# Performance work log

Hardware: AMD Instinct MI355X
Metric: run time of the kernel (lower is better)

Reference implementation:

```python
import jax, jax.numpy as jnp
import numpy as np

N = 100000   # nodes
E = 50000    # hyperedges
K = 4        # nodes per hyperedge
D = 128      # out_dim (= in_dim here)
ED = 64      # edge_dim
H = 8        # num_heads


def _build_pairs(seed=0):
    # Sparse equivalent of the incidence-matrix nested loops:
    # for each edge e with member set S, emit ordered pairs (v, e, u) for v,u in S.
    rng = np.random.default_rng(seed)
    cover = rng.permutation(N).reshape(N // K, K)          # guarantees every node owns >=1 pair group
    rand = rng.integers(0, N, size=(E - N // K, K))
    edge_nodes = np.concatenate([cover, rand], axis=0)      # [E, K]
    owners = np.repeat(edge_nodes, K, axis=1).ravel()       # v, repeated K times per edge slot
    pair_u = np.tile(edge_nodes, (1, K)).ravel()            # u, tiled
    pair_e = np.repeat(np.arange(E), K * K)
    return owners.astype(np.int32), pair_e.astype(np.int32), pair_u.astype(np.int32)


def setup_inputs() -> dict:
    key = jax.random.key(0)
    ks = jax.random.split(key, 12)
    owners, pair_e, pair_u = _build_pairs()
    s = 0.05
    return {
        "x": jax.random.normal(ks[0], (N, D), jnp.float32),
        "edge_attr": jax.random.normal(ks[1], (E, ED), jnp.float32),
        "w_lin": jax.random.normal(ks[2], (D, D), jnp.float32) * s,   # self.lin (no bias)
        "w_e": jax.random.normal(ks[3], (ED, D), jnp.float32) * s,    # self.edge_lin (no bias)
        "w_q": jax.random.normal(ks[4], (D, D), jnp.float32) * s,
        "b_q": jax.random.normal(ks[5], (D,), jnp.float32) * s,
        "w_k": jax.random.normal(ks[6], (D, D), jnp.float32) * s,
        "b_k": jax.random.normal(ks[7], (D,), jnp.float32) * s,
        "w_v": jax.random.normal(ks[8], (D, D), jnp.float32) * s,
        "b_v": jax.random.normal(ks[9], (D,), jnp.float32) * s,
        "w_o": jax.random.normal(ks[10], (D, D), jnp.float32) * s,
        "b_o": jax.random.normal(ks[11], (D,), jnp.float32) * s,
        "owners": jnp.asarray(owners),
        "pair_e": jnp.asarray(pair_e),
        "pair_u": jnp.asarray(pair_u),
    }


def reference(x, edge_attr, w_lin, w_e, w_q, b_q, w_k, b_k, w_v, b_v, w_o, b_o, owners, pair_e, pair_u):
    n = x.shape[0]
    d = w_lin.shape[1]
    dh = d // H
    Wh = x @ w_lin                                  # [N, D]
    We = edge_attr @ w_e                            # [E, D]
    # Multi-head single-query attention per node over its (e,u) pair set.
    q = ((Wh @ w_q + b_q) / jnp.sqrt(jnp.asarray(dh, Wh.dtype))).reshape(n, H, dh)
    Wh_u = Wh[pair_u]                               # [P, D] value source (= Wh[u])
    k = ((Wh_u + We[pair_e]) @ w_k + b_k).reshape(-1, H, dh)   # key source = Wh[u] + We[e]
    v = (Wh_u @ w_v + b_v).reshape(-1, H, dh)
    scores = jnp.einsum('phd,phd->ph', q[owners], k)            # [P, H]
    # segmented (ragged) softmax over each node's pair set
    m = jax.ops.segment_max(scores, owners, num_segments=n)
    ex = jnp.exp(scores - m[owners])
    denom = jax.ops.segment_sum(ex, owners, num_segments=n)     # [N, H]
    alpha = ex / denom[owners]                                  # [P, H]
    ctx = jax.ops.segment_sum(alpha[..., None] * v, owners, num_segments=n).reshape(n, d)
    out = ctx @ w_o + b_o
    return jax.nn.relu(out)
```

## Files before the change

### kernel.cpp

```cpp
#include <hip/hip_runtime.h>

#define NN 100000
#define EE 50000
#define GG (EE*4)
#define CAP 24

#define QKV_BLOCKS 1563
#define KE_BLOCKS  1564
#define BKT_BLOCKS 782

typedef __attribute__((ext_vector_type(8))) short bf16x8;
typedef __attribute__((ext_vector_type(4))) float f32x4;

__device__ __forceinline__ unsigned short f2bf(float f) {
  union { float f; unsigned int u; } c; c.f = f;
  unsigned int u = c.u;
  u = (u + 0x7fffu + ((u >> 16) & 1u)) >> 16;
  return (unsigned short)u;
}
__device__ __forceinline__ float bf2f(unsigned int lo16) {
  union { unsigned int u; float f; } c; c.u = lo16 << 16;
  return c.f;
}
__device__ __forceinline__ bf16x8 pack8(const float* f) {
  union { bf16x8 v; unsigned int u[4]; } r;
  #pragma unroll
  for (int i = 0; i < 4; ++i)
    r.u[i] = (unsigned int)f2bf(f[2*i]) | ((unsigned int)f2bf(f[2*i+1]) << 16);
  return r.v;
}

struct __align__(8) us4 { unsigned short x, y, z, w; };

__global__ void k_prep(const float* __restrict__ w_lin, const float* __restrict__ w_e,
                       const float* __restrict__ w_q, const float* __restrict__ b_q,
                       const float* __restrict__ w_k, const float* __restrict__ b_k,
                       const float* __restrict__ w_v, const float* __restrict__ b_v,
                       const float* __restrict__ w_o, const float* __restrict__ b_o,
                       unsigned short* __restrict__ WT, unsigned short* __restrict__ WeT,
                       unsigned short* __restrict__ WoT, float* __restrict__ bias384,
                       float* __restrict__ bkB, float* __restrict__ boB) {
  int t = blockIdx.x * 256 + threadIdx.x;
  if (t < 49152) {
    int sel = t >> 14, k = (t >> 7) & 127, nn = t & 127;
    const float* wsel = sel == 0 ? w_q : (sel == 1 ? w_k : w_v);
    float scale = sel == 0 ? 0.25f : 1.0f;
    float s = 0.f;
    for (int d = 0; d < 128; ++d)
      s += w_lin[k*128 + d] * wsel[d*128 + nn];
    WT[(size_t)(sel * 128 + nn) * 128 + k] = f2bf(s * scale);
  } else if (t < 57344) {
    int i = t - 49152, k = i >> 7, nn = i & 127;
    float s = 0.f;
    for (int d = 0; d < 128; ++d)
      s += w_e[k*128 + d] * w_k[d*128 + nn];
    WeT[nn*64 + k] = f2bf(s);
  } else if (t < 73728) {
    int i = t - 57344, k = i >> 7, n = i & 127;
    WoT[n*128 + k] = f2bf(w_o[k*128 + n]);
  } else if (t < 74112) {
    int i = t - 73728;
    bias384[i] = (i < 128) ? b_q[i] * 0.25f : ((i < 256) ? 0.f : b_v[i - 256]);
  } else if (t < 74240) {
    bkB[t - 74112] = b_k[t - 74112];
  } else if (t < 74368) {
    boB[t - 74240] = b_o[t - 74240];
  }
}

__global__ __launch_bounds__(256) void k_mid(const float* __restrict__ x,
                                             const unsigned short* __restrict__ WT,
                                             const float* __restrict__ bias,
                                             unsigned short* __restrict__ qkv,
                                             const float* __restrict__ ea,
                                             const unsigned short* __restrict__ WeT,
                                             const float* __restrict__ bk,
                                             unsigned short* __restrict__ ke,
                                             const int* __restrict__ owners,
                                             int* __restrict__ cnt,
                                             int* __restrict__ glist) {
  __shared__ unsigned short lds[64 * 144];
  int bid = blockIdx.x;
  int tid = threadIdx.x;

  if (bid < QKV_BLOCKS) {
    unsigned short* As = lds;
    int row0 = bid * 64;
    #pragma unroll
    for (int it = 0; it < 8; ++it) {
      int i4 = tid + it * 256;
      int r = i4 >> 5, c4 = i4 & 31;
      float4 vv = make_float4(0.f, 0.f, 0.f, 0.f);
      int gr = row0 + r;
      if (gr < NN) vv = *(const float4*)(x + (size_t)gr * 128 + c4 * 4);
      us4 s4 = { f2bf(vv.x), f2bf(vv.y), f2bf(vv.z), f2bf(vv.w) };
      int chunk = c4 >> 1;
      int soff = r * 128 + ((chunk ^ (r & 7)) << 3) + ((c4 & 1) << 2);
      *(us4*)(&As[soff]) = s4;
    }
    __syncthreads();
    int w = tid >> 6, lane = tid & 63, lr = lane & 15, lk = lane >> 4;
    bf16x8 afr[4][4];
    #pragma unroll
    for (int rt = 0; rt < 4; ++rt) {
      int R = rt * 16 + lr;
      #pragma unroll
      for (int kk = 0; kk < 4; ++kk) {
        int chunk = (kk * 4 + lk) ^ (R & 7);
        afr[rt][kk] = *(const bf16x8*)(&As[R * 128 + chunk * 8]);
      }
    }
    #pragma unroll
    for (int p = 0; p < 3; ++p) {
      f32x4 acc[2][4] = {};
      #pragma unroll
      for (int h = 0; h < 2; ++h) {
        int gcol = p * 128 + h * 64 + w * 16 + lr;
        const unsigned short* bp = WT + (size_t)gcol * 128 + lk * 8;
        bf16x8 b0 = *(const bf16x8*)(bp);
        bf16x8 b1 = *(const bf16x8*)(bp + 32);
        bf16x8 b2 = *(const bf16x8*)(bp + 64);
        bf16x8 b3 = *(const bf16x8*)(bp + 96);
        #pragma unroll
        for (int rt = 0; rt < 4; ++rt) {
          acc[h][rt] = __builtin_amdgcn_mfma_f32_16x16x32_bf16(afr[rt][0], b0, acc[h][rt], 0, 0, 0);
          acc[h][rt] = __builtin_amdgcn_mfma_f32_16x16x32_bf16(afr[rt][1], b1, acc[h][rt], 0, 0, 0);
          acc[h][rt] = __builtin_amdgcn_mfma_f32_16x16x32_bf16(afr[rt][2], b2, acc[h][rt], 0, 0, 0);
          acc[h][rt] = __builtin_amdgcn_mfma_f32_16x16x32_bf16(afr[rt][3], b3, acc[h][rt], 0, 0, 0);
        }
      }
      __syncthreads();
      #pragma unroll
      for (int h = 0; h < 2; ++h) {
        int colp = h * 64 + w * 16 + lr;
        float b = bias[p * 128 + colp];
        #pragma unroll
        for (int rt = 0; rt < 4; ++rt) {
          #pragma unroll
          for (int j = 0; j < 4; ++j) {
            As[(rt * 16 + lk * 4 + j) * 136 + colp] = f2bf(acc[h][rt][j] + b);
          }
        }
      }
      __syncthreads();
      int piece = tid & 15, rbase = tid >> 4;
      #pragma unroll
      for (int it = 0; it < 4; ++it) {
        int r = rbase + it * 16;
        int grow = row0 + r;
        if (grow < NN) {
          float4 vv = *(const float4*)(&As[r * 136 + piece * 8]);
          *(float4*)(qkv + (size_t)grow * 384 + p * 128 + piece * 8) = vv;
        }
      }
    }
  } else if (bid < QKV_BLOCKS + KE_BLOCKS) {
    int idx = bid - QKV_BLOCKS;
    int row0 = (idx % 782) * 64;
    int col0 = (idx / 782) * 64;
    unsigned short* As = lds;
    unsigned short* Bs = lds + 64 * 72;
    #pragma unroll
    for (int it = 0; it < 4; ++it) {
      int i4 = tid + it * 256;
      int r = i4 >> 4, c4 = i4 & 15;
      float4 vv = make_float4(0.f, 0.f, 0.f, 0.f);
      int gr = row0 + r;
      if (gr < EE) vv = *(const float4*)(ea + (size_t)gr * 64 + c4 * 4);
      us4 s4 = { f2bf(vv.x), f2bf(vv.y), f2bf(vv.z), f2bf(vv.w) };
      *(us4*)(&As[r * 72 + c4 * 4]) = s4;
    }
    #pragma unroll
    for (int it = 0; it < 4; ++it) {
      int i4 = tid + it * 256;
      int r = i4 >> 4, c4 = i4 & 15;
      us4 s4 = *(const us4*)(WeT + (size_t)(col0 + r) * 64 + c4 * 4);
      *(us4*)(&Bs[r * 72 + c4 * 4]) = s4;
    }
    __syncthreads();
    int w = tid >> 6, lane = tid & 63, lr = lane & 15, lk = lane >> 4;
    f32x4 acc[4] = {};
    #pragma unroll
    for (int kk = 0; kk < 2; ++kk) {
      int kof = kk * 32 + lk * 8;
      bf16x8 af = *(const bf16x8*)(&As[(w * 16 + lr) * 72 + kof]);
      #pragma unroll
      for (int nt = 0; nt < 4; ++nt) {
        bf16x8 bfrag = *(const bf16x8*)(&Bs[(nt * 16 + lr) * 72 + kof]);
        acc[nt] = __builtin_amdgcn_mfma_f32_16x16x32_bf16(af, bfrag, acc[nt], 0, 0, 0);
      }
    }
    #pragma unroll
    for (int nt = 0; nt < 4; ++nt) {
      int gcol = col0 + nt * 16 + lr;
      float b = bk[gcol];
      #pragma unroll
      for (int j = 0; j < 4; ++j) {
        int grow = row0 + w * 16 + lk * 4 + j;
        if (grow < EE) ke[(size_t)grow * 128 + gcol] = f2bf(acc[nt][j] + b);
      }
    }
  } else {
    int g = (bid - QKV_BLOCKS - KE_BLOCKS) * 256 + tid;
    if (g < GG) {
      int v = owners[(size_t)g * 4];
      int p = atomicAdd(cnt + v, 1);
      if (p < CAP) glist[(size_t)v * CAP + p] = g;
    }
  }
}

__global__ __launch_bounds__(256) void k_edge(const unsigned short* __restrict__ qkv,
                                              const unsigned short* __restrict__ ke,
                                              const int* __restrict__ pair_u,
                                              unsigned short* __restrict__ pctx,
                                              float* __restrict__ pden) {
  int e0 = (blockIdx.x * 4 + (threadIdx.x >> 6)) * 4;
  if (e0 >= EE) return;
  int lane = threadIdx.x & 63;
  int m[4][4];
  #pragma unroll
  for (int ee = 0; ee < 4; ++ee)
    #pragma unroll
    for (int j = 0; j < 4; ++j)
      m[ee][j] = __builtin_amdgcn_readfirstlane(pair_u[(size_t)(e0 + ee) * 16 + j]);
  unsigned int kew[4];
  #pragma unroll
  for (int ee = 0; ee < 4; ++ee)
    kew[ee] = *(const unsigned int*)(ke + (size_t)(e0 + ee) * 128 + 2 * lane);
  unsigned int qw[4][4], kw[4][4], vw[4][4];
  #pragma unroll
  for (int ee = 0; ee < 4; ++ee)
    #pragma unroll
    for (int j = 0; j < 4; ++j) {
      const unsigned short* r = qkv + (size_t)m[ee][j] * 384 + 2 * lane;
      qw[ee][j] = *(const unsigned int*)r;
      kw[ee][j] = *(const unsigned int*)(r + 128);
      vw[ee][j] = *(const unsigned int*)(r + 256);
    }
  #pragma unroll
  for (int ee = 0; ee < 4; ++ee) {
    float e0f = bf2f(kew[ee] & 0xffffu), e1f = bf2f(kew[ee] >> 16);
    float qa[4][2], ka[4][2], va[4][2];
    #pragma unroll
    for (int j = 0; j < 4; ++j) {
      qa[j][0] = bf2f(qw[ee][j] & 0xffffu);        qa[j][1] = bf2f(qw[ee][j] >> 16);
      ka[j][0] = bf2f(kw[ee][j] & 0xffffu) + e0f;  ka[j][1] = bf2f(kw[ee][j] >> 16) + e1f;
      va[j][0] = bf2f(vw[ee][j] & 0xffffu);        va[j][1] = bf2f(vw[ee][j] >> 16);
    }
    #pragma unroll
    for (int i = 0; i < 4; ++i) {
      float c0 = 0.f, c1 = 0.f, ds = 0.f;
      #pragma unroll
      for (int j = 0; j < 4; ++j) {
        float sc = qa[i][0] * ka[j][0] + qa[i][1] * ka[j][1];
        sc += __shfl_xor(sc, 1);
        sc += __shfl_xor(sc, 2);
        sc += __shfl_xor(sc, 4);
        float ex = __expf(sc);
        c0 += ex * va[j][0];
        c1 += ex * va[j][1];
        ds += ex;
      }
      int slot = (e0 + ee) * 4 + i;
      unsigned int packed = (unsigned int)f2bf(c0) | ((unsigned int)f2bf(c1) << 16);
      *(unsigned int*)(pctx + (size_t)slot * 128 + 2 * lane) = packed;
      if ((lane & 7) == 0) pden[(size_t)slot * 8 + (lane >> 3)] = ds;
    }
  }
}

__global__ __launch_bounds__(256) void k_out(const unsigned short* __restrict__ pctx,
                                             const float* __restrict__ pden,
                                             const int* __restrict__ cnt,
                                             const int* __restrict__ glist,
                                             const unsigned short* __restrict__ WoT,
                                             const float* __restrict__ bo,
                                             float* __restrict__ out) {
  int wid = blockIdx.x * 4 + (threadIdx.x >> 6);
  if (wid >= NN / 32) return;
  int lane = threadIdx.x & 63, lr = lane & 15, lk = lane >> 4;
  int rowA = wid * 32 + lr, rowB = rowA + 16;
  float aA[4][8], aB[4][8];
  float dsA[4] = { 0.f, 0.f, 0.f, 0.f }, dsB[4] = { 0.f, 0.f, 0.f, 0.f };
  #pragma unroll
  for (int kk = 0; kk < 4; ++kk)
    #pragma unroll
    for (int i = 0; i < 8; ++i) { aA[kk][i] = 0.f; aB[kk][i] = 0.f; }
  int cA = cnt[rowA]; if (cA > CAP) cA = CAP;
  int cB = cnt[rowB]; if (cB > CAP) cB = CAP;
  int iA = 0, iB = 0;
  for (;;) {
    bool doA = iA < cA, doB = iB < cB;
    if (!__any((int)(doA || doB))) break;
    if (doA) {
      int sl = glist[(size_t)rowA * CAP + iA];
      const unsigned short* pr = pctx + (size_t)sl * 128 + lk * 8;
      const float* dp = pden + (size_t)sl * 8 + (lk >> 1);
      #pragma unroll
      for (int kk = 0; kk < 4; ++kk) {
        uint4 v = *(const uint4*)(pr + kk * 32);
        aA[kk][0] += bf2f(v.x & 0xffffu); aA[kk][1] += bf2f(v.x >> 16);
        aA[kk][2] += bf2f(v.y & 0xffffu); aA[kk][3] += bf2f(v.y >> 16);
        aA[kk][4] += bf2f(v.z & 0xffffu); aA[kk][5] += bf2f(v.z >> 16);
        aA[kk][6] += bf2f(v.w & 0xffffu); aA[kk][7] += bf2f(v.w >> 16);
        dsA[kk] += dp[kk * 2];
      }
      ++iA;
    }
    if (doB) {
      int sl = glist[(size_t)rowB * CAP + iB];
      const unsigned short* pr = pctx + (size_t)sl * 128 + lk * 8;
      const float* dp = pden + (size_t)sl * 8 + (lk >> 1);
      #pragma unroll
      for (int kk = 0; kk < 4; ++kk) {
        uint4 v = *(const uint4*)(pr + kk * 32);
        aB[kk][0] += bf2f(v.x & 0xffffu); aB[kk][1] += bf2f(v.x >> 16);
        aB[kk][2] += bf2f(v.y & 0xffffu); aB[kk][3] += bf2f(v.y >> 16);
        aB[kk][4] += bf2f(v.z & 0xffffu); aB[kk][5] += bf2f(v.z >> 16);
        aB[kk][6] += bf2f(v.w & 0xffffu); aB[kk][7] += bf2f(v.w >> 16);
        dsB[kk] += dp[kk * 2];
      }
      ++iB;
    }
  }
  bf16x8 abfA[4], abfB[4];
  #pragma unroll
  for (int kk = 0; kk < 4; ++kk) {
    float invA = dsA[kk] > 0.f ? 1.0f / dsA[kk] : 0.f;
    float invB = dsB[kk] > 0.f ? 1.0f / dsB[kk] : 0.f;
    float fA[8], fB[8];
    #pragma unroll
    for (int i = 0; i < 8; ++i) { fA[i] = aA[kk][i] * invA; fB[i] = aB[kk][i] * invB; }
    abfA[kk] = pack8(fA);
    abfB[kk] = pack8(fB);
  }
  #pragma unroll
  for (int ct = 0; ct < 8; ++ct) {
    const unsigned short* wp = WoT + (size_t)(ct * 16 + lr) * 128 + lk * 8;
    bf16x8 w0 = *(const bf16x8*)(wp);
    bf16x8 w1 = *(const bf16x8*)(wp + 32);
    bf16x8 w2 = *(const bf16x8*)(wp + 64);
    bf16x8 w3 = *(const bf16x8*)(wp + 96);
    f32x4 accA = {}, accB = {};
    accA = __builtin_amdgcn_mfma_f32_16x16x32_bf16(w0, abfA[0], accA, 0, 0, 0);
    accA = __builtin_amdgcn_mfma_f32_16x16x32_bf16(w1, abfA[1], accA, 0, 0, 0);
    accA = __builtin_amdgcn_mfma_f32_16x16x32_bf16(w2, abfA[2], accA, 0, 0, 0);
    accA = __builtin_amdgcn_mfma_f32_16x16x32_bf16(w3, abfA[3], accA, 0, 0, 0);
    accB = __builtin_amdgcn_mfma_f32_16x16x32_bf16(w0, abfB[0], accB, 0, 0, 0);
    accB = __builtin_amdgcn_mfma_f32_16x16x32_bf16(w1, abfB[1], accB, 0, 0, 0);
    accB = __builtin_amdgcn_mfma_f32_16x16x32_bf16(w2, abfB[2], accB, 0, 0, 0);
    accB = __builtin_amdgcn_mfma_f32_16x16x32_bf16(w3, abfB[3], accB, 0, 0, 0);
    float4 bb = *(const float4*)(bo + ct * 16 + lk * 4);
    float4 oA, oB;
    oA.x = fmaxf(accA[0] + bb.x, 0.f); oA.y = fmaxf(accA[1] + bb.y, 0.f);
    oA.z = fmaxf(accA[2] + bb.z, 0.f); oA.w = fmaxf(accA[3] + bb.w, 0.f);
    oB.x = fmaxf(accB[0] + bb.x, 0.f); oB.y = fmaxf(accB[1] + bb.y, 0.f);
    oB.z = fmaxf(accB[2] + bb.z, 0.f); oB.w = fmaxf(accB[3] + bb.w, 0.f);
    *(float4*)(out + (size_t)rowA * 128 + ct * 16 + lk * 4) = oA;
    *(float4*)(out + (size_t)rowB * 128 + ct * 16 + lk * 4) = oB;
  }
}

extern "C" void kernel_launch(void* const* d_in, const int* in_sizes, int n_in,
                              void* d_out, int out_size, void* d_ws, size_t ws_size,
                              hipStream_t stream) {
  const float* x      = (const float*)d_in[0];
  const float* ea     = (const float*)d_in[1];
  const float* w_lin  = (const float*)d_in[2];
  const float* w_e    = (const float*)d_in[3];
  const float* w_q    = (const float*)d_in[4];
  const float* b_q    = (const float*)d_in[5];
  const float* w_k    = (const float*)d_in[6];
  const float* b_k    = (const float*)d_in[7];
  const float* w_v    = (const float*)d_in[8];
  const float* b_v    = (const float*)d_in[9];
  const float* w_o    = (const float*)d_in[10];
  const float* b_o    = (const float*)d_in[11];
  const int* owners   = (const int*)d_in[12];
  const int* pair_u   = (const int*)d_in[14];
  float* out = (float*)d_out;

  char* base = (char*)d_ws;
  size_t o = 0;
  auto alloc = [&](size_t b) {
    void* p = base + o;
    o = (o + b + 255) & ~(size_t)255;
    return p;
  };
  unsigned short* WT      = (unsigned short*)alloc((size_t)384 * 128 * 2);
  unsigned short* WeT     = (unsigned short*)alloc((size_t)128 * 64 * 2);
  unsigned short* WoT     = (unsigned short*)alloc((size_t)128 * 128 * 2);
  float* bias384          = (float*)alloc(384 * 4);
  float* bkB              = (float*)alloc(128 * 4);
  float* boB              = (float*)alloc(128 * 4);
  unsigned short* qkv     = (unsigned short*)alloc((size_t)NN * 384 * 2);
  unsigned short* keb     = (unsigned short*)alloc((size_t)EE * 128 * 2);
  int* cnt                = (int*)alloc((size_t)NN * 4);
  int* glist              = (int*)alloc((size_t)NN * CAP * 4);
  unsigned short* pctx    = (unsigned short*)alloc((size_t)GG * 128 * 2);
  float* pden             = (float*)alloc((size_t)GG * 8 * 4);

  hipMemsetAsync(cnt, 0, (size_t)NN * 4, stream);

  k_prep<<<291, 256, 0, stream>>>(w_lin, w_e, w_q, b_q, w_k, b_k, w_v, b_v, w_o, b_o,
                                  WT, WeT, WoT, bias384, bkB, boB);
  k_mid<<<QKV_BLOCKS + KE_BLOCKS + BKT_BLOCKS, 256, 0, stream>>>(
      x, WT, bias384, qkv, ea, WeT, bkB, keb, owners, cnt, glist);
  k_edge<<<3125, 256, 0, stream>>>(qkv, keb, pair_u, pctx, pden);
  k_out<<<782, 256, 0, stream>>>(pctx, pden, cnt, glist, WoT, boB, out);
}
```

Baseline: 152.4 us.

## Split QKV GEMM per wave into row/column halves with per-wave epilogue staging

Each wave in the QKV projection blocks now computes a 32-row by 192-column sub-tile instead of all 64 rows by a column slice. Its output goes through a private padded LDS staging buffer, so the epilogue needs no block-wide __syncthreads. This removes the two barriers per output panel and halves the A-fragment registers per wave. In exchange, each wave loads twice as many weight fragments, global stores are narrower per row, and the 16-byte LDS reads at a 34-element stride are not 16-byte aligned.

```diff
diff --git a/kernel.cpp b/kernel.cpp
--- a/kernel.cpp
+++ b/kernel.cpp
@@ -79,7 +79,7 @@
                                              const int* __restrict__ owners,
                                              int* __restrict__ cnt,
                                              int* __restrict__ glist) {
-  __shared__ unsigned short lds[64 * 144];
+  __shared__ unsigned short lds[64 * 128 + 4 * 32 * 34];
   int bid = blockIdx.x;
   int tid = threadIdx.x;
 
@@ -100,58 +100,55 @@
     }
     __syncthreads();
     int w = tid >> 6, lane = tid & 63, lr = lane & 15, lk = lane >> 4;
-    bf16x8 afr[4][4];
-    #pragma unroll
-    for (int rt = 0; rt < 4; ++rt) {
-      int R = rt * 16 + lr;
+    int rhalf = w >> 1;
+    int chalf = w & 1;
+    bf16x8 afr[2][4];
+    #pragma unroll
+    for (int rt = 0; rt < 2; ++rt) {
+      int R = rhalf * 32 + rt * 16 + lr;
       #pragma unroll
       for (int kk = 0; kk < 4; ++kk) {
         int chunk = (kk * 4 + lk) ^ (R & 7);
         afr[rt][kk] = *(const bf16x8*)(&As[R * 128 + chunk * 8]);
       }
     }
-    #pragma unroll
-    for (int p = 0; p < 3; ++p) {
-      f32x4 acc[2][4] = {};
-      #pragma unroll
-      for (int h = 0; h < 2; ++h) {
-        int gcol = p * 128 + h * 64 + w * 16 + lr;
-        const unsigned short* bp = WT + (size_t)gcol * 128 + lk * 8;
+    unsigned short* sw = lds + 64 * 128 + w * (32 * 34);
+    int rd = lane >> 1, cb = (lane & 1) * 16;
+    #pragma unroll
+    for (int ct0 = 0; ct0 < 12; ct0 += 2) {
+      f32x4 acc[2][2] = {};
+      float bb[2];
+      #pragma unroll
+      for (int sub = 0; sub < 2; ++sub) {
+        int c = chalf * 12 + ct0 + sub;
+        const unsigned short* bp = WT + (size_t)(c * 16 + lr) * 128 + lk * 8;
         bf16x8 b0 = *(const bf16x8*)(bp);
         bf16x8 b1 = *(const bf16x8*)(bp + 32);
         bf16x8 b2 = *(const bf16x8*)(bp + 64);
         bf16x8 b3 = *(const bf16x8*)(bp + 96);
+        bb[sub] = bias[c * 16 + lr];
         #pragma unroll
-        for (int rt = 0; rt < 4; ++rt) {
-          acc[h][rt] = __builtin_amdgcn_mfma_f32_16x16x32_bf16(afr[rt][0], b0, acc[h][rt], 0, 0, 0);
-          acc[h][rt] = __builtin_amdgcn_mfma_f32_16x16x32_bf16(afr[rt][1], b1, acc[h][rt], 0, 0, 0);
-          acc[h][rt] = __builtin_amdgcn_mfma_f32_16x16x32_bf16(afr[rt][2], b2, acc[h][rt], 0, 0, 0);
-          acc[h][rt] = __builtin_amdgcn_mfma_f32_16x16x32_bf16(afr[rt][3], b3, acc[h][rt], 0, 0, 0);
+        for (int rt = 0; rt < 2; ++rt) {
+          acc[sub][rt] = __builtin_amdgcn_mfma_f32_16x16x32_bf16(afr[rt][0], b0, acc[sub][rt], 0, 0, 0);
+          acc[sub][rt] = __builtin_amdgcn_mfma_f32_16x16x32_bf16(afr[rt][1], b1, acc[sub][rt], 0, 0, 0);
+          acc[sub][rt] = __builtin_amdgcn_mfma_f32_16x16x32_bf16(afr[rt][2], b2, acc[sub][rt], 0, 0, 0);
+          acc[sub][rt] = __builtin_amdgcn_mfma_f32_16x16x32_bf16(afr[rt][3], b3, acc[sub][rt], 0, 0, 0);
         }
       }
-      __syncthreads();
-      #pragma unroll
-      for (int h = 0; h < 2; ++h) {
-        int colp = h * 64 + w * 16 + lr;
-        float b = bias[p * 128 + colp];
+      #pragma unroll
+      for (int sub = 0; sub < 2; ++sub)
         #pragma unroll
-        for (int rt = 0; rt < 4; ++rt) {
+        for (int rt = 0; rt < 2; ++rt)
           #pragma unroll
-          for (int j = 0; j < 4; ++j) {
-            As[(rt * 16 + lk * 4 + j) * 136 + colp] = f2bf(acc[h][rt][j] + b);
-          }
-        }
-      }
-      __syncthreads();
-      int piece = tid & 15, rbase = tid >> 4;
-      #pragma unroll
-      for (int it = 0; it < 4; ++it) {
-        int r = rbase + it * 16;
-        int grow = row0 + r;
-        if (grow < NN) {
-          float4 vv = *(const float4*)(&As[r * 136 + piece * 8]);
-          *(float4*)(qkv + (size_t)grow * 384 + p * 128 + piece * 8) = vv;
-        }
+          for (int j = 0; j < 4; ++j)
+            sw[(rt * 16 + lk * 4 + j) * 34 + sub * 16 + lr] = f2bf(acc[sub][rt][j] + bb[sub]);
+      int grow = row0 + rhalf * 32 + rd;
+      if (grow < NN) {
+        float4 v0 = *(const float4*)(&sw[rd * 34 + cb]);
+        float4 v1 = *(const float4*)(&sw[rd * 34 + cb + 8]);
+        size_t go = (size_t)grow * 384 + chalf * 192 + ct0 * 16 + cb;
+        *(float4*)(qkv + go) = v0;
+        *(float4*)(qkv + go + 8) = v1;
       }
     }
   } else if (bid < QKV_BLOCKS + KE_BLOCKS) {
```

Result: slower. 166.3 us (+9.1%).
